# Performance work log

Hardware: AMD Instinct MI355X
Metric: run time of the kernel (lower is better)

The kernel has to match this reference:

```python
import jax, jax.numpy as jnp
import numpy as np

N, H, E, K = 256, 128, 64, 4  # nodes, hidden, dist-embed dim, heads
ALPHA = 0.2  # leaky-relu slope


def setup_inputs() -> dict:
    key = jax.random.key(0)
    ks = jax.random.split(key, 12)
    s = lambda k, sh: (jax.random.normal(k, sh, jnp.float32) * 0.05)
    return dict(
        action_hidden_state=jax.random.normal(ks[0], (N, H), jnp.float32),
        goal_hidden_state=jax.random.normal(ks[1], (N, H), jnp.float32),
        goal=jax.random.normal(ks[2], (N, 2), jnp.float32),
        action=jax.random.normal(ks[3], (N, 2), jnp.float32),
        W_emb=s(ks[4], (1, E)), b_emb=jnp.zeros((E,), jnp.float32),
        W_gate=s(ks[5], (2 * E + 2 * H, H)), b_gate=jnp.zeros((H,), jnp.float32),
        W_gat=s(ks[6], (K, H, H)), a_src=s(ks[7], (K, H)), a_dst=s(ks[8], (K, H)),
        gat_bias=jnp.zeros((H,), jnp.float32),
    )


def cal_dist(goal, action):
    # Vectorized, math-faithful (incl. source typos) version of the O(n^2) loop.
    ax, ay = action[:, 0], action[:, 1]
    gx, gy = goal[:, 0], goal[:, 1]
    a1x, a1y = ax[:, None], ay[:, None]   # node i
    a2x, a2y = ax[None, :], ay[None, :]   # node j
    g1x, g1y = gx[:, None], gy[:, None]
    g2x, g2y = gx[None, :], gy[None, :]
    dn = (a1x - a1x) * (g1y - g2y) - (a1y - a2y) * (g1x - g2x)
    cross_a = a1x * a2y - a1y * a2x
    gterm = g1x * g2y - g1x * g2x
    n1 = cross_a * (g1x - g2x) - (a1x - a2x) * gterm
    n2 = cross_a * (g1y - g2y) - (a1y - a2x) * gterm
    safe = jnp.where(dn == 0.0, 1.0, dn)
    p1, p2 = n1 / safe, n2 / safe
    base = jnp.linalg.norm(action - goal, axis=-1)  # [n]
    d1p = jnp.sqrt((a1x - p1) ** 2 + (a1y - p2) ** 2)
    d2p = jnp.sqrt((a2x - p1) ** 2 + (a2y - p2) ** 2)
    cond = (dn != 0.0) & ((a1x - p1) * (p1 - g1x) > 0.0)
    ones = jnp.ones_like(dn)
    d1 = jnp.where(cond, d1p, base[:, None] * ones)
    d2 = jnp.where(cond, d2p, base[None, :] * ones)
    n = d1.shape[0]
    ii = jnp.arange(n)[:, None]
    jj = jnp.arange(n)[None, :]
    # dist[i,j]=d1(i,j) for i<j; dist[j,i]=d2(i,j) i.e. lower triangle = d2.T; diag = |a_i - g_i|
    return jnp.where(ii == jj, base[:, None] * ones, jnp.where(ii < jj, d1, d2.T))


def reference(action_hidden_state, goal_hidden_state, goal, action,
              W_emb, b_emb, W_gate, b_gate, W_gat, a_src, a_dst, gat_bias):
    ha, hg = action_hidden_state, goal_hidden_state
    n, h = ha.shape
    dist = cal_dist(goal, action)                      # [n,n]
    emb = dist[..., None] * W_emb[0] + b_emb           # Linear(1,E) -> [n,n,E]
    # pairwise interaction gate (i != idx branch, computed for all pairs)
    gate_in = jnp.concatenate([
        jnp.broadcast_to(ha[:, None, :], (n, n, h)),
        jnp.broadcast_to(ha[None, :, :], (n, n, h)),
        emb, jnp.swapaxes(emb, 0, 1)], axis=-1)        # [n,n,2H+2E]
    gate = jax.nn.sigmoid(gate_in @ W_gate + b_gate)   # [n,n,H]
    gated = ha[None, :, :] * gate
    # self branch: gates the goal hidden state; action row stays ungated
    emb_d = emb[jnp.arange(n), jnp.arange(n)]          # [n,E]
    gate_self = jax.nn.sigmoid(
        jnp.concatenate([ha, hg, emb_d, emb_d], axis=-1) @ W_gate + b_gate)
    curr_goal = hg * gate_self                         # [n,H]
    eye = jnp.eye(n, dtype=bool)[..., None]
    curr_action = jnp.where(eye, ha[:, None, :], gated)          # [n,n,H]
    gat_in = jnp.concatenate([curr_action, curr_goal[:, None, :]], axis=1)  # [n,n+1,H]
    # multi-head GAT layer (batched over the n query nodes)
    hp = jnp.einsum('bmf,kfo->bkmo', gat_in, W_gat)    # [n,K,m,H]
    attn = (jnp.einsum('bkmo,ko->bkm', hp, a_src)[..., :, None]
            + jnp.einsum('bkmo,ko->bkm', hp, a_dst)[..., None, :])  # [n,K,m,m]
    attn = jax.nn.softmax(jax.nn.leaky_relu(attn, ALPHA), axis=-1)
    out = jnp.einsum('bkij,bkjo->bkio', attn, hp).mean(axis=1) + gat_bias  # [n,m,H]
    out = jax.nn.elu(out)
    idx = jnp.arange(n)
    return out[idx, idx]                               # [n,H]
```

## Files before the change

kernel.cpp:

```cpp
#include <hip/hip_runtime.h>
#include <math.h>

#define N 256
#define H 128
#define E 64
#define K 4
#define M (N + 1)
#define WAVES 16
#define BLOCK 1024

__device__ __forceinline__ float sigm(float x) {
    return __fdividef(1.0f, 1.0f + __expf(-x));
}

__device__ __forceinline__ float wave_sum(float v) {
#pragma unroll
    for (int d = 1; d < 64; d <<= 1) v += __shfl_xor(v, d, 64);
    return v;
}

__device__ __forceinline__ float readlane_f(float v, int l) {
    return __uint_as_float(__builtin_amdgcn_readlane(__float_as_uint(v), l));
}

__device__ __forceinline__ float kbutterfly(float q0, float q1, float q2, float q3,
                                            int lane) {
    const bool b1 = lane & 1;
    const bool b2 = lane & 2;
    float aA = b1 ? q1 : q0, aB = b1 ? q0 : q1;
    aA += __shfl_xor(aB, 1, 64);
    float cA = b1 ? q3 : q2, cB = b1 ? q2 : q3;
    cA += __shfl_xor(cB, 1, 64);
    float eA = b2 ? cA : aA, eB = b2 ? aA : cA;
    eA += __shfl_xor(eB, 2, 64);
#pragma unroll
    for (int d = 4; d < 64; d <<= 1) eA += __shfl_xor(eA, d, 64);
    return eA;
}

__device__ __forceinline__ void pairdist(
    float a1x, float a1y, float a2x, float a2y,
    float g1x, float g1y, float g2x, float g2y,
    float baseR, float baseC, float& d_rc, float& d_cr)
{
    float t  = __fmul_rn(__fsub_rn(a1y, a2y), __fsub_rn(g1x, g2x));
    float dn = -t;
    float ca = __fsub_rn(__fmul_rn(a1x, a2y), __fmul_rn(a1y, a2x));
    float gt = __fsub_rn(__fmul_rn(g1x, g2y), __fmul_rn(g1x, g2x));
    float n1 = __fsub_rn(__fmul_rn(ca, __fsub_rn(g1x, g2x)),
                         __fmul_rn(__fsub_rn(a1x, a2x), gt));
    float n2 = __fsub_rn(__fmul_rn(ca, __fsub_rn(g1y, g2y)),
                         __fmul_rn(__fsub_rn(a1y, a2x), gt));
    float safe = (dn == 0.0f) ? 1.0f : dn;
    float p1 = __fdiv_rn(n1, safe);
    float p2 = __fdiv_rn(n2, safe);
    bool cond = (dn != 0.0f) &&
                (__fmul_rn(__fsub_rn(a1x, p1), __fsub_rn(p1, g1x)) > 0.0f);
    float dx1 = __fsub_rn(a1x, p1), dy1 = __fsub_rn(a1y, p2);
    float d1p = __fsqrt_rn(__fadd_rn(__fmul_rn(dx1, dx1), __fmul_rn(dy1, dy1)));
    float dx2 = __fsub_rn(a2x, p1), dy2 = __fsub_rn(a2y, p2);
    float d2p = __fsqrt_rn(__fadd_rn(__fmul_rn(dx2, dx2), __fmul_rn(dy2, dy2)));
    d_rc = cond ? d1p : baseR;
    d_cr = cond ? d2p : baseC;
}

__global__ __launch_bounds__(BLOCK) void gat_pre(
    const float* __restrict__ ha, const float* __restrict__ hg,
    const float* __restrict__ W_emb, const float* __restrict__ b_emb,
    const float* __restrict__ W_gate, const float* __restrict__ b_gate,
    const float* __restrict__ W_gat, const float* __restrict__ a_src,
    const float* __restrict__ a_dst,
    float* __restrict__ A1, float* __restrict__ G2,
    float* __restrict__ u3g, float* __restrict__ u4g, float* __restrict__ ccg,
    float* __restrict__ vsrc, float* __restrict__ vdst,
    float4* __restrict__ pk)
{
    const int b    = blockIdx.x;
    const int tid  = threadIdx.x;
    const int wid  = tid >> 6;
    const int lane = tid & 63;

    __shared__ float sRed[8][3][H];
    __shared__ float sA2[H];
    __shared__ float sU[8][3][64];

    {
        const int f  = tid & (H - 1);
        const int sl = tid >> 7;
        const int g0 = sl * 16;
        float s1 = 0.f, s2 = 0.f, s3 = 0.f;
#pragma unroll
        for (int g = 0; g < 16; ++g) {
            const int gg = g0 + g;
            float w1 = W_gate[gg * H + f];
            float w2 = W_gate[(H + gg) * H + f];
            float av = ha[b * H + gg];
            float gv = hg[b * H + gg];
            s1 += av * w1;
            s2 += av * w2;
            s3 += gv * w2;
        }
        sRed[sl][0][f] = s1;
        sRed[sl][1][f] = s2;
        sRed[sl][2][f] = s3;
    }

    if (wid >= 14) {
        const int p = 2 * b + (wid - 14);
        const int k = p >> 7;
        const int f = p & (H - 1);
        const float2 w2 = ((const float2*)&W_gat[(k * H + f) * H])[lane];
        const float2 as2 = ((const float2*)&a_src[k * H])[lane];
        const float2 ad2 = ((const float2*)&a_dst[k * H])[lane];
        float vsv = wave_sum(w2.x * as2.x + w2.y * as2.y);
        float vdv = wave_sum(w2.x * ad2.x + w2.y * ad2.y);
        if (lane == 0) { vsrc[k * H + f] = vsv; vdst[k * H + f] = vdv; }
    }

    if (b < 2 && wid >= 2 && wid < 10) {
        const int sl = wid - 2;
        const int f  = (b << 6) | lane;
        float s3 = 0.f, s4 = 0.f, scc = 0.f;
#pragma unroll
        for (int e0 = 0; e0 < 8; ++e0) {
            const int e = sl * 8 + e0;
            float w3 = W_gate[(2 * H + e) * H + f];
            float w4 = W_gate[(2 * H + E + e) * H + f];
            float we = W_emb[e], be = b_emb[e];
            s3  += we * w3;
            s4  += we * w4;
            scc += be * (w3 + w4);
        }
        sU[sl][0][lane] = s3;
        sU[sl][1][lane] = s4;
        sU[sl][2][lane] = scc;
    }
    __syncthreads();

    if (tid < H) {
        float r1 = 0.f, r2 = 0.f, r3 = 0.f;
#pragma unroll
        for (int sl = 0; sl < 8; ++sl) {
            r1 += sRed[sl][0][tid];
            r2 += sRed[sl][1][tid];
            r3 += sRed[sl][2][tid];
        }
        A1[b * H + tid] = r1;
        G2[b * H + tid] = r3;
        sA2[tid] = r2;
    }
    __syncthreads();

    if (tid < 64) {
        const float2 h2 = ((const float2*)&ha[b * H])[tid];
        pk[(b << 6) | tid] = make_float4(sA2[2 * tid], sA2[2 * tid + 1], h2.x, h2.y);
    }
    if (b < 2 && tid < 192) {
        const int c  = tid >> 6;
        const int fl = tid & 63;
        float r = 0.f;
#pragma unroll
        for (int w = 0; w < 8; ++w) r += sU[w][c][fl];
        const int f = (b << 6) | fl;
        if (c == 0)      u3g[f] = r;
        else if (c == 1) u4g[f] = r;
        else             ccg[f] = r + b_gate[f];
    }
}

__global__ __launch_bounds__(BLOCK) void gat_main(
    const float* __restrict__ ha, const float* __restrict__ hg,
    const float* __restrict__ W_gat, const float* __restrict__ gat_bias,
    const float* __restrict__ A1, const float* __restrict__ G2,
    const float* __restrict__ u3a, const float* __restrict__ u4a,
    const float* __restrict__ cca,
    const float* __restrict__ vsrc, const float* __restrict__ vdst,
    const float4* __restrict__ pk,
    const float* __restrict__ goal, const float* __restrict__ action,
    float* __restrict__ out)
{
    const int i    = blockIdx.x;
    const int tid  = threadIdx.x;
    const int wid  = tid >> 6;
    const int lane = tid & 63;
    const int f0   = lane * 2;

    __shared__ float2 sAct[N];
    __shared__ float2 sGoal[N];
    __shared__ float  sBase[N];
    __shared__ float2 sD[M];
    __shared__ float  sW[WAVES][K][H];
    __shared__ float  sL[WAVES][K];
    __shared__ float  sWfin[K][H];
    __shared__ float  sPart[8][H];

    const float2 a1v = *(const float2*)&A1[i * H + f0];
    const float2 haI = *(const float2*)&ha[i * H + f0];
    const float2 hgI = *(const float2*)&hg[i * H + f0];
    const float2 g2v = *(const float2*)&G2[i * H + f0];
    const float2 u3  = *(const float2*)&u3a[f0];
    const float2 u4  = *(const float2*)&u4a[f0];
    const float2 cc  = *(const float2*)&cca[f0];
    const float2 vd0 = *(const float2*)&vdst[0 * H + f0];
    const float2 vd1 = *(const float2*)&vdst[1 * H + f0];
    const float2 vd2 = *(const float2*)&vdst[2 * H + f0];
    const float2 vd3 = *(const float2*)&vdst[3 * H + f0];
    const float2 vs0 = *(const float2*)&vsrc[0 * H + f0];
    const float2 vs1 = *(const float2*)&vsrc[1 * H + f0];
    const float2 vs2 = *(const float2*)&vsrc[2 * H + f0];
    const float2 vs3 = *(const float2*)&vsrc[3 * H + f0];

    if (tid < N) {
        float2 a = ((const float2*)action)[tid];
        float2 g = ((const float2*)goal)[tid];
        sAct[tid]  = a;
        sGoal[tid] = g;
        float dx = __fsub_rn(a.x, g.x), dy = __fsub_rn(a.y, g.y);
        sBase[tid] = __fsqrt_rn(__fadd_rn(__fmul_rn(dx, dx), __fmul_rn(dy, dy)));
    }
    __syncthreads();

    if (tid < M) {
        const int j = tid;
        float dij = 0.f, dji = 0.f;
        if (j != i && j != N) {
            const float2 aI = sAct[i], gI = sGoal[i];
            const float2 aJ = sAct[j], gJ = sGoal[j];
            if (i < j)
                pairdist(aI.x, aI.y, aJ.x, aJ.y, gI.x, gI.y, gJ.x, gJ.y,
                         sBase[i], sBase[j], dij, dji);
            else
                pairdist(aJ.x, aJ.y, aI.x, aI.y, gJ.x, gJ.y, gI.x, gI.y,
                         sBase[j], sBase[i], dji, dij);
        }
        sD[j] = make_float2(dij, dji);
    }

    const float scOwn = kbutterfly(haI.x * vs0.x + haI.y * vs0.y,
                                   haI.x * vs1.x + haI.y * vs1.y,
                                   haI.x * vs2.x + haI.y * vs2.y,
                                   haI.x * vs3.x + haI.y * vs3.y, lane);

    const float2 a1cc = make_float2(a1v.x + cc.x, a1v.y + cc.y);
    const float baseI = sBase[i];
    __syncthreads();

    float l_ = 0.f;
    float w00 = 0.f, w01 = 0.f, w02 = 0.f, w03 = 0.f;
    float w10 = 0.f, w11 = 0.f, w12 = 0.f, w13 = 0.f;

#pragma unroll
    for (int t = 0; t < 16; ++t) {
        const int jj = wid + 16 * t;
        const float4 ph = pk[(jj << 6) | lane];
        const float2 d  = sD[jj];
        float tx = a1cc.x + ph.x + d.x * u3.x + d.y * u4.x;
        float ty = a1cc.y + ph.y + d.x * u3.y + d.y * u4.y;
        float2 g = make_float2(ph.z * sigm(tx), ph.w * sigm(ty));
        if (jj == i) g = haI;

        float q0 = g.x * vd0.x + g.y * vd0.y;
        float q1 = g.x * vd1.x + g.y * vd1.y;
        float q2 = g.x * vd2.x + g.y * vd2.y;
        float q3 = g.x * vd3.x + g.y * vd3.y;
        float e  = kbutterfly(q0, q1, q2, q3, lane);

        float lg = scOwn + e;
        lg = (lg >= 0.f) ? lg : 0.2f * lg;
        const float p = __expf(lg);
        l_ += p;

        const float p0 = readlane_f(p, 0), p1 = readlane_f(p, 1);
        const float p2 = readlane_f(p, 2), p3 = readlane_f(p, 3);
        w00 += p0 * g.x;  w10 += p0 * g.y;
        w01 += p1 * g.x;  w11 += p1 * g.y;
        w02 += p2 * g.x;  w12 += p2 * g.y;
        w03 += p3 * g.x;  w13 += p3 * g.y;
    }

    if (wid == 0) {
        float tx = a1cc.x + g2v.x + baseI * (u3.x + u4.x);
        float ty = a1cc.y + g2v.y + baseI * (u3.y + u4.y);
        float2 g = make_float2(hgI.x * sigm(tx), hgI.y * sigm(ty));

        float q0 = g.x * vd0.x + g.y * vd0.y;
        float q1 = g.x * vd1.x + g.y * vd1.y;
        float q2 = g.x * vd2.x + g.y * vd2.y;
        float q3 = g.x * vd3.x + g.y * vd3.y;
        float e  = kbutterfly(q0, q1, q2, q3, lane);

        float lg = scOwn + e;
        lg = (lg >= 0.f) ? lg : 0.2f * lg;
        const float p = __expf(lg);
        l_ += p;

        const float p0 = readlane_f(p, 0), p1 = readlane_f(p, 1);
        const float p2 = readlane_f(p, 2), p3 = readlane_f(p, 3);
        w00 += p0 * g.x;  w10 += p0 * g.y;
        w01 += p1 * g.x;  w11 += p1 * g.y;
        w02 += p2 * g.x;  w12 += p2 * g.y;
        w03 += p3 * g.x;  w13 += p3 * g.y;
    }

    *(float2*)&sW[wid][0][f0] = make_float2(w00, w10);
    *(float2*)&sW[wid][1][f0] = make_float2(w01, w11);
    *(float2*)&sW[wid][2][f0] = make_float2(w02, w12);
    *(float2*)&sW[wid][3][f0] = make_float2(w03, w13);
    if (lane < K) sL[wid][lane] = l_;
    __syncthreads();

    if (tid < K * H) {
        const int k = tid >> 7;
        const int f = tid & (H - 1);
        float W = 0.f;
#pragma unroll
        for (int w = 0; w < WAVES; ++w) W += sW[w][k][f];
        float L = 0.f;
#pragma unroll
        for (int w = 0; w < WAVES; ++w) L += sL[w][k];
        sWfin[k][f] = W / L;
    }
    __syncthreads();

    {
        const int f = tid & (H - 1);
        const int s = tid >> 7;
        float acc = 0.0f;
#pragma unroll
        for (int k = 0; k < K; ++k) {
            const int g0 = s * 16;
#pragma unroll
            for (int g = 0; g < 16; ++g)
                acc += sWfin[k][g0 + g] * W_gat[(k * H + g0 + g) * H + f];
        }
        sPart[s][f] = acc;
    }
    __syncthreads();

    if (tid < H) {
        float acc = 0.0f;
#pragma unroll
        for (int s = 0; s < 8; ++s) acc += sPart[s][tid];
        float val = 0.25f * acc + gat_bias[tid];
        out[i * H + tid] = (val > 0.0f) ? val : expm1f(val);
    }
}

extern "C" void kernel_launch(void* const* d_in, const int* in_sizes, int n_in,
                              void* d_out, int out_size, void* d_ws, size_t ws_size,
                              hipStream_t stream)
{
    const float* ha       = (const float*)d_in[0];
    const float* hg       = (const float*)d_in[1];
    const float* goal     = (const float*)d_in[2];
    const float* action   = (const float*)d_in[3];
    const float* W_emb    = (const float*)d_in[4];
    const float* b_emb    = (const float*)d_in[5];
    const float* W_gate   = (const float*)d_in[6];
    const float* b_gate   = (const float*)d_in[7];
    const float* W_gat    = (const float*)d_in[8];
    const float* a_src    = (const float*)d_in[9];
    const float* a_dst    = (const float*)d_in[10];
    const float* gat_bias = (const float*)d_in[11];

    float* ws  = (float*)d_ws;
    float*  A1 = ws;
    float*  G2 = A1 + N * H;
    float*  u3 = G2 + N * H;
    float*  u4 = u3 + H;
    float*  cc = u4 + H;
    float*  vs = cc + H;
    float*  vd = vs + K * H;
    float4* pk = (float4*)(vd + K * H);

    hipLaunchKernelGGL(gat_pre, dim3(N), dim3(BLOCK), 0, stream,
                       ha, hg, W_emb, b_emb, W_gate, b_gate,
                       W_gat, a_src, a_dst,
                       A1, G2, u3, u4, cc, vs, vd, pk);

    hipLaunchKernelGGL(gat_main, dim3(N), dim3(BLOCK), 0, stream,
                       ha, hg, W_gat, gat_bias,
                       A1, G2, u3, u4, cc, vs, vd, pk,
                       goal, action, (float*)d_out);
}
```

Baseline: 26.50 us.

## Compute pair distances per wave in registers, dropping shared staging and barriers

In the main kernel, each wave now computes the 16 pair distances it needs in lanes 0-15, reading action and goal straight from global memory. Each loop iteration then broadcasts its distance with readlane instead of reading it from shared memory. This removes two block-wide __syncthreads and the shared arrays for action, goal, base and distances, at the cost of recomputing base norms per lane. The prep kernel also spreads its final reduction across 384 threads instead of 128.

```diff
diff --git a/kernel.cpp b/kernel.cpp
--- a/kernel.cpp
+++ b/kernel.cpp
@@ -36,6 +36,11 @@
 #pragma unroll
     for (int d = 4; d < 64; d <<= 1) eA += __shfl_xor(eA, d, 64);
     return eA;
+}
+
+__device__ __forceinline__ float base_of(float2 a, float2 g) {
+    float dx = __fsub_rn(a.x, g.x), dy = __fsub_rn(a.y, g.y);
+    return __fsqrt_rn(__fadd_rn(__fmul_rn(dx, dx), __fmul_rn(dy, dy)));
 }
 
 __device__ __forceinline__ void pairdist(
@@ -137,17 +142,15 @@
     }
     __syncthreads();
 
-    if (tid < H) {
-        float r1 = 0.f, r2 = 0.f, r3 = 0.f;
-#pragma unroll
-        for (int sl = 0; sl < 8; ++sl) {
-            r1 += sRed[sl][0][tid];
-            r2 += sRed[sl][1][tid];
-            r3 += sRed[sl][2][tid];
-        }
-        A1[b * H + tid] = r1;
-        G2[b * H + tid] = r3;
-        sA2[tid] = r2;
+    if (tid < 3 * H) {
+        const int c = tid >> 7;
+        const int f = tid & (H - 1);
+        float r = 0.f;
+#pragma unroll
+        for (int sl = 0; sl < 8; ++sl) r += sRed[sl][c][f];
+        if (c == 0)      A1[b * H + f] = r;
+        else if (c == 2) G2[b * H + f] = r;
+        else             sA2[f] = r;
     }
     __syncthreads();
 
@@ -185,14 +188,10 @@
     const int lane = tid & 63;
     const int f0   = lane * 2;
 
-    __shared__ float2 sAct[N];
-    __shared__ float2 sGoal[N];
-    __shared__ float  sBase[N];
-    __shared__ float2 sD[M];
-    __shared__ float  sW[WAVES][K][H];
-    __shared__ float  sL[WAVES][K];
-    __shared__ float  sWfin[K][H];
-    __shared__ float  sPart[8][H];
+    __shared__ float sW[WAVES][K][H];
+    __shared__ float sL[WAVES][K];
+    __shared__ float sWfin[K][H];
+    __shared__ float sPart[8][H];
 
     const float2 a1v = *(const float2*)&A1[i * H + f0];
     const float2 haI = *(const float2*)&ha[i * H + f0];
@@ -210,30 +209,23 @@
     const float2 vs2 = *(const float2*)&vsrc[2 * H + f0];
     const float2 vs3 = *(const float2*)&vsrc[3 * H + f0];
 
-    if (tid < N) {
-        float2 a = ((const float2*)action)[tid];
-        float2 g = ((const float2*)goal)[tid];
-        sAct[tid]  = a;
-        sGoal[tid] = g;
-        float dx = __fsub_rn(a.x, g.x), dy = __fsub_rn(a.y, g.y);
-        sBase[tid] = __fsqrt_rn(__fadd_rn(__fmul_rn(dx, dx), __fmul_rn(dy, dy)));
-    }
-    __syncthreads();
-
-    if (tid < M) {
-        const int j = tid;
-        float dij = 0.f, dji = 0.f;
-        if (j != i && j != N) {
-            const float2 aI = sAct[i], gI = sGoal[i];
-            const float2 aJ = sAct[j], gJ = sGoal[j];
+    float dijv = 0.f, djiv = 0.f;
+    if (lane < 16) {
+        const int j = wid + 16 * lane;
+        if (j != i) {
+            const float2 aI = ((const float2*)action)[i];
+            const float2 gI = ((const float2*)goal)[i];
+            const float2 aJ = ((const float2*)action)[j];
+            const float2 gJ = ((const float2*)goal)[j];
+            const float bI = base_of(aI, gI);
+            const float bJ = base_of(aJ, gJ);
             if (i < j)
                 pairdist(aI.x, aI.y, aJ.x, aJ.y, gI.x, gI.y, gJ.x, gJ.y,
-                         sBase[i], sBase[j], dij, dji);
+                         bI, bJ, dijv, djiv);
             else
                 pairdist(aJ.x, aJ.y, aI.x, aI.y, gJ.x, gJ.y, gI.x, gI.y,
-                         sBase[j], sBase[i], dji, dij);
+                         bJ, bI, djiv, dijv);
         }
-        sD[j] = make_float2(dij, dji);
     }
 
     const float scOwn = kbutterfly(haI.x * vs0.x + haI.y * vs0.y,
@@ -242,8 +234,6 @@
                                    haI.x * vs3.x + haI.y * vs3.y, lane);
 
     const float2 a1cc = make_float2(a1v.x + cc.x, a1v.y + cc.y);
-    const float baseI = sBase[i];
-    __syncthreads();
 
     float l_ = 0.f;
     float w00 = 0.f, w01 = 0.f, w02 = 0.f, w03 = 0.f;
@@ -253,9 +243,10 @@
     for (int t = 0; t < 16; ++t) {
         const int jj = wid + 16 * t;
         const float4 ph = pk[(jj << 6) | lane];
-        const float2 d  = sD[jj];
-        float tx = a1cc.x + ph.x + d.x * u3.x + d.y * u4.x;
-        float ty = a1cc.y + ph.y + d.x * u3.y + d.y * u4.y;
+        const float dx = readlane_f(dijv, t);
+        const float dy = readlane_f(djiv, t);
+        float tx = a1cc.x + ph.x + dx * u3.x + dy * u4.x;
+        float ty = a1cc.y + ph.y + dx * u3.y + dy * u4.y;
         float2 g = make_float2(ph.z * sigm(tx), ph.w * sigm(ty));
         if (jj == i) g = haI;
 
@@ -279,6 +270,9 @@
     }
 
     if (wid == 0) {
+        const float2 aI = ((const float2*)action)[i];
+        const float2 gI = ((const float2*)goal)[i];
+        const float baseI = base_of(aI, gI);
         float tx = a1cc.x + g2v.x + baseI * (u3.x + u4.x);
         float ty = a1cc.y + g2v.y + baseI * (u3.y + u4.y);
         float2 g = make_float2(hgI.x * sigm(tx), hgI.y * sigm(ty));
```

After: 26.60 us. About the same (+0.4%).
